# Performance work log

Measured on AMD Instinct MI355X. Metric: run time of the kernel, lower is better.

Reference implementation:

```python
import jax, jax.numpy as jnp
import numpy as np

B = 128                      # num_graphs (cell lines per batch)
SIZES = [706, 512, 256, 128] # nodes per graph at each level; final_node = 128
DIM = 256                    # dim_cell
DEG = 8                      # avg degree of gene-gene network
EPS = 1e-5                   # BatchNorm eps


def _build_graph():
    """Build per-graph edges (incl. self-loops, as GATConv adds) and predefined
    cluster assignments per layer, coarsening edges exactly like PyG max_pool
    (remove self-loops + coalesce). Replicated across B graphs with offsets."""
    rng = np.random.default_rng(0)
    e = rng.integers(0, SIZES[0], size=(2, SIZES[0] * DEG))
    e = e[:, e[0] != e[1]]
    e = np.unique(e, axis=1)
    edges, clusters = [], []
    cur = e
    for i in range(3):
        n_cur, n_next = SIZES[i], SIZES[i + 1]
        sl = np.arange(n_cur)
        e_sl = np.concatenate([cur, np.stack([sl, sl])], axis=1)  # add self-loops
        off = np.arange(B) * n_cur
        eg = (e_sl[:, None, :] + off[None, :, None]).reshape(2, -1)
        edges.append(eg.astype(np.int32))
        cl = np.concatenate([np.arange(n_next), rng.integers(0, n_next, size=n_cur - n_next)])
        rng.shuffle(cl)  # surjective cluster assignment n_cur -> n_next
        clg = (cl[None, :] + (np.arange(B) * n_next)[:, None]).reshape(-1)
        clusters.append(clg.astype(np.int32))
        src, dst = cl[cur[0]], cl[cur[1]]
        m = src != dst                      # pool_edge: remove self-loops
        cur = np.unique(np.stack([src[m], dst[m]]), axis=1)  # coalesce
    return edges, clusters


def setup_inputs() -> dict:
    edges, clusters = _build_graph()
    key = jax.random.key(0)
    ks = jax.random.split(key, 16)
    d = {"x": jax.random.normal(ks[0], (B * SIZES[0], 3), jnp.float32)}
    ins = [3, DIM, DIM]
    for i in range(3):
        s = 1.0 / np.sqrt(ins[i])
        a = 1.0 / np.sqrt(DIM)
        d[f"W{i}"] = jax.random.normal(ks[1 + i], (ins[i], DIM), jnp.float32) * s
        d[f"asrc{i}"] = jax.random.normal(ks[4 + i], (DIM,), jnp.float32) * a
        d[f"adst{i}"] = jax.random.normal(ks[7 + i], (DIM,), jnp.float32) * a
        d[f"b{i}"] = jnp.zeros((DIM,), jnp.float32)
        d[f"edge{i}"] = jnp.asarray(edges[i])
        d[f"cluster{i}"] = jnp.asarray(clusters[i])
    return d


def _gat(x, edge, W, a_s, a_d, b):
    """PyG GATConv, heads=1, negative_slope=0.2 (self-loops pre-added in edge)."""
    N = x.shape[0]
    h = x @ W                                    # [N, D]
    src, dst = edge[0], edge[1]
    e = jax.nn.leaky_relu((h * a_s).sum(-1)[src] + (h * a_d).sum(-1)[dst], 0.2)
    m = jax.ops.segment_max(e, dst, num_segments=N)     # segment softmax (stable)
    ex = jnp.exp(e - m[dst])
    ssum = jax.ops.segment_sum(ex, dst, num_segments=N)
    alpha = ex / ssum[dst]
    out = jax.ops.segment_sum(h[src] * alpha[:, None], dst, num_segments=N)
    return out + b


def _forward(x, Ws, a_ss, a_ds, bs, edges, clusters):
    for i in range(3):
        x = jax.nn.relu(_gat(x, edges[i], Ws[i], a_ss[i], a_ds[i], bs[i]))
        # max_pool: scatter-max over predefined clusters (coarsen nodes)
        x = jax.ops.segment_max(x, clusters[i], num_segments=B * SIZES[i + 1])
        # BatchNorm1d(affine=False), training mode: biased batch stats
        mean = x.mean(0)
        var = x.var(0)
        x = (x - mean) * jax.lax.rsqrt(var + EPS)
    return x.reshape(B, SIZES[3] * DIM)


def reference(x, W0, W1, W2, asrc0, asrc1, asrc2, adst0, adst1, adst2,
              b0, b1, b2, edge0, edge1, edge2, cluster0, cluster1, cluster2):
    return _forward(x, (W0, W1, W2), (asrc0, asrc1, asrc2), (adst0, adst1, adst2),
                    (b0, b1, b2), (edge0, edge1, edge2), (cluster0, cluster1, cluster2))
```

## Files before the change

### kernel.cpp

```cpp
#include <hip/hip_runtime.h>
#include <hip/hip_fp16.h>

#define DIM 256
#define MAXMEM 16
#define MAXDEG 288
#define NSH 16

typedef _Float16 f16x8 __attribute__((ext_vector_type(8)));
typedef float f32x4 __attribute__((ext_vector_type(4)));

__device__ inline unsigned short f2h(float f) {
  return __half_as_ushort(__float2half_rn(f));
}
__device__ inline float h2f(unsigned short u) {
  return __half2float(__ushort_as_half(u));
}
__device__ inline __half2 hmax2_(__half2 a, __half2 b) {
  __half2 c;
  c.x = __hgt(a.x, b.x) ? a.x : b.x;
  c.y = __hgt(a.y, b.y) ? a.y : b.y;
  return c;
}


struct BktArgs {
  const int* esrc[3]; const int* edst[3]; const int* cl[3];
  int Eb[3]; int Nb[3]; int est[3];
  int* bdeg[3]; int* bccnt[3]; int* bebkt[3]; int* bcbkt[3];
};

__global__ __launch_bounds__(256) void l0_bucket(
    const float* __restrict__ x, const float* __restrict__ W,
    const float* __restrict__ asv, const float* __restrict__ adv,
    unsigned short* __restrict__ h, float* __restrict__ ssrc,
    float* __restrict__ sdst, int N, int Nb0, int l0Blocks, int bgx,
    BktArgs a) {
  if ((int)blockIdx.x >= l0Blocks) {
    int bb = blockIdx.x - l0Blocks;
    int L = bb / bgx;
    int i = (bb % bgx) * 256 + threadIdx.x;
    if (i < a.Eb[L]) {
      int d = a.edst[L][i];
      int slot = atomicAdd(&a.bdeg[L][d], 1);
      if (slot < a.est[L]) a.bebkt[L][d * a.est[L] + slot] = a.esrc[L][i];
    }
    if (i < a.Nb[L]) {
      int c = a.cl[L][i];
      int slot = atomicAdd(&a.bccnt[L][c], 1);
      if (slot < MAXMEM) a.bcbkt[L][c * MAXMEM + slot] = i;
    }
    return;
  }
  int wid = (blockIdx.x * 256 + threadIdx.x) >> 6;
  int lane = threadIdx.x & 63;
  if (wid >= N) return;
  int nb = wid >> 7, g = wid & 127;
  const float* xr = x + ((size_t)g * Nb0 + nb) * 3;
  float x0 = xr[0], x1 = xr[1], x2 = xr[2];
  int c = lane * 4;
  float4 w0 = *(const float4*)(W + c);
  float4 w1 = *(const float4*)(W + 256 + c);
  float4 w2 = *(const float4*)(W + 512 + c);
  float4 hv;
  hv.x = fmaf(x0, w0.x, fmaf(x1, w1.x, x2 * w2.x));
  hv.y = fmaf(x0, w0.y, fmaf(x1, w1.y, x2 * w2.y));
  hv.z = fmaf(x0, w0.z, fmaf(x1, w1.z, x2 * w2.z));
  hv.w = fmaf(x0, w0.w, fmaf(x1, w1.w, x2 * w2.w));
  ((ushort4*)(h + (size_t)wid * DIM))[lane] =
      make_ushort4(f2h(hv.x), f2h(hv.y), f2h(hv.z), f2h(hv.w));
  float4 a1 = ((const float4*)asv)[lane];
  float4 a2 = ((const float4*)adv)[lane];
  float d1 = hv.x * a1.x + hv.y * a1.y + hv.z * a1.z + hv.w * a1.w;
  float d2 = hv.x * a2.x + hv.y * a2.y + hv.z * a2.z + hv.w * a2.w;
  for (int o = 32; o > 0; o >>= 1) {
    d1 += __shfl_down(d1, o);
    d2 += __shfl_down(d2, o);
  }
  if (lane == 0) { ssrc[wid] = d1; sdst[wid] = d2; }
}

__global__ __launch_bounds__(256) void prep_k(
    const float* __restrict__ W, const float* __restrict__ stats,
    float invN, unsigned short* __restrict__ Wt, float* __restrict__ cvec) {
  int n = blockIdx.x;
  int k = threadIdx.x;
  float s = 0.f, q = 0.f;
#pragma unroll
  for (int sh = 0; sh < NSH; sh++) {
    s += stats[sh * 512 + k];
    q += stats[sh * 512 + 256 + k];
  }
  float mu = s * invN;
  float var = q * invN - mu * mu;
  float istd = rsqrtf(var + 1e-5f);
  float w = W[(size_t)k * 256 + n] * istd;
  Wt[(size_t)n * 256 + k] = f2h(w);
  __shared__ float red[256];
  red[k] = mu * w;
  __syncthreads();
  for (int sft = 128; sft > 0; sft >>= 1) {
    if (k < sft) red[k] += red[k + sft];
    __syncthreads();
  }
  if (k == 0) cvec[n] = -red[0];
}

__global__ __launch_bounds__(256) void gemm_mfma(
    const unsigned short* __restrict__ A, const unsigned short* __restrict__ Wt,
    const float* __restrict__ cvec, const float* __restrict__ asv,
    const float* __restrict__ adv, unsigned short* __restrict__ H,
    float* __restrict__ ssrc, float* __restrict__ sdst, int M) {
  __shared__ unsigned short Bs[256 * 128];
  int tid = threadIdx.x;
  int wave = tid >> 6, lane = tid & 63;
  int m0 = blockIdx.x * 128 + wave * 32;
  int row = lane & 15, quad = lane >> 4;
  int swz = (row & 7) << 3;

  const unsigned short* Ap = A + (size_t)(m0 + row) * 256 + quad * 8;
  f32x4 acc[2][16] = {};

#pragma unroll
  for (int kh = 0; kh < 2; kh++) {
    if (kh) __syncthreads();
#pragma unroll
    for (int k = 0; k < 16; k++) {
      int c = k * 256 + tid;
      f16x8 v = *(const f16x8*)(const void*)(Wt + (size_t)(c >> 4) * 256 +
                                             kh * 128 + (c & 15) * 8);
      *(f16x8*)(void*)(&Bs[(c * 8) ^ (((c >> 4) & 7) << 3)]) = v;
    }
    __syncthreads();
#pragma unroll
    for (int j2 = 0; j2 < 4; j2++) {
      int j = kh * 4 + j2;
      f16x8 a0 = *(const f16x8*)(const void*)(Ap + j * 32);
      f16x8 a1 = *(const f16x8*)(const void*)(Ap + 16 * 256 + j * 32);
#pragma unroll
      for (int nt = 0; nt < 16; nt++) {
        f16x8 b = *(const f16x8*)(const void*)(
            &Bs[((nt * 16 + row) * 128 + j2 * 32 + quad * 8) ^ swz]);
        acc[0][nt] = __builtin_amdgcn_mfma_f32_16x16x32_f16(a0, b, acc[0][nt], 0, 0, 0);
        acc[1][nt] = __builtin_amdgcn_mfma_f32_16x16x32_f16(a1, b, acc[1][nt], 0, 0, 0);
      }
    }
  }

  float sav[16], sdv[16], cv[16];
#pragma unroll
  for (int nt = 0; nt < 16; nt++) {
    sav[nt] = asv[nt * 16 + row];
    sdv[nt] = adv[nt * 16 + row];
    cv[nt] = cvec[nt * 16 + row];
  }
#pragma unroll
  for (int sub = 0; sub < 2; sub++)
#pragma unroll
    for (int r = 0; r < 4; r++) {
      int mm = m0 + sub * 16 + quad * 4 + r;
      unsigned short* out = H + (size_t)mm * 256 + row;
      float d1 = 0.f, d2 = 0.f;
#pragma unroll
      for (int nt = 0; nt < 16; nt++) {
        float hv = acc[sub][nt][r] + cv[nt];
        out[nt * 16] = f2h(hv);
        d1 = fmaf(hv, sav[nt], d1);
        d2 = fmaf(hv, sdv[nt], d2);
      }
      for (int o = 1; o < 16; o <<= 1) {
        d1 += __shfl_xor(d1, o);
        d2 += __shfl_xor(d2, o);
      }
      if (row == 0) { ssrc[mm] = d1; sdst[mm] = d2; }
    }
}

__global__ __launch_bounds__(256) void gat_fused(
    const unsigned short* __restrict__ h, const int* __restrict__ bdeg,
    const int* __restrict__ bebkt, int estride,
    const int* __restrict__ bccnt, const int* __restrict__ bcbkt,
    const float* __restrict__ ssrc, const float* __restrict__ sdst,
    const float* __restrict__ bias, unsigned short* __restrict__ pooled,
    int Mb, int lgMb) {
  __shared__ float pLDS[MAXDEG * 8];
  __shared__ float psum[8];
  int b = blockIdx.x;
  int x = b & 7, t = b >> 3;
  int c = t & (Mb - 1);
  int set = x + 8 * (t >> lgMb);
  int tid = threadIdx.x;
  int gl = tid >> 5;
  int ch = tid & 31;
  int g = set * 8 + gl;
  int nm = bccnt[c]; if (nm > MAXMEM) nm = MAXMEM;
  float4 bf0 = *(const float4*)(bias + ch * 8);
  float4 bf1 = *(const float4*)(bias + ch * 8 + 4);
  __half2 hb[4] = {__floats2half2_rn(bf0.x, bf0.y), __floats2half2_rn(bf0.z, bf0.w),
                   __floats2half2_rn(bf1.x, bf1.y), __floats2half2_rn(bf1.z, bf1.w)};
  __half2 z = __float2half2_rn(0.f);
  __half2 best[4] = {z, z, z, z};
  for (int mi = 0; mi < nm; mi++) {
    int nb = __builtin_amdgcn_readfirstlane(bcbkt[c * MAXMEM + mi]);
    int deg = __builtin_amdgcn_readfirstlane(bdeg[nb]);
    if (deg > estride) deg = estride;
    const int* bk = bebkt + nb * estride;
    if (tid < 8) psum[tid] = 0.f;
    __syncthreads();
    for (int jj = tid; jj < deg * 8; jj += 256) {
      int j = jj >> 3, gi = jj & 7;
      int g2 = set * 8 + gi;
      int s = bk[j];
      float tt = ssrc[s * 128 + g2] + sdst[nb * 128 + g2];
      tt = tt > 0.f ? tt : 0.2f * tt;
      float p = __expf(tt);
      pLDS[jj] = p;
      atomicAdd(&psum[gi], p);
    }
    __syncthreads();
    float inv = 1.f / psum[gl];
    __half2 acc[4] = {z, z, z, z};
    int j = 0;
    for (; j + 4 <= deg; j += 4) {
      int4 ss = *(const int4*)(bk + j);
      __half2 hq0 = __float2half2_rn(pLDS[(j + 0) * 8 + gl] * inv);
      __half2 hq1 = __float2half2_rn(pLDS[(j + 1) * 8 + gl] * inv);
      __half2 hq2 = __float2half2_rn(pLDS[(j + 2) * 8 + gl] * inv);
      __half2 hq3 = __float2half2_rn(pLDS[(j + 3) * 8 + gl] * inv);
      uint4 v0 = *(const uint4*)(h + ((size_t)ss.x * 128 + g) * DIM + ch * 8);
      uint4 v1 = *(const uint4*)(h + ((size_t)ss.y * 128 + g) * DIM + ch * 8);
      uint4 v2 = *(const uint4*)(h + ((size_t)ss.z * 128 + g) * DIM + ch * 8);
      uint4 v3 = *(const uint4*)(h + ((size_t)ss.w * 128 + g) * DIM + ch * 8);
      union { uint4 u; __half2 p[4]; } u0, u1, u2, u3;
      u0.u = v0; u1.u = v1; u2.u = v2; u3.u = v3;
#pragma unroll
      for (int i = 0; i < 4; i++) {
        acc[i] = __hfma2(u0.p[i], hq0, acc[i]);
        acc[i] = __hfma2(u1.p[i], hq1, acc[i]);
        acc[i] = __hfma2(u2.p[i], hq2, acc[i]);
        acc[i] = __hfma2(u3.p[i], hq3, acc[i]);
      }
    }
    for (; j < deg; j++) {
      int s = bk[j];
      __half2 hq = __float2half2_rn(pLDS[j * 8 + gl] * inv);
      uint4 v0 = *(const uint4*)(h + ((size_t)s * 128 + g) * DIM + ch * 8);
      union { uint4 u; __half2 p[4]; } u0; u0.u = v0;
#pragma unroll
      for (int i = 0; i < 4; i++) acc[i] = __hfma2(u0.p[i], hq, acc[i]);
    }
#pragma unroll
    for (int i = 0; i < 4; i++)
      best[i] = hmax2_(best[i], __hadd2(acc[i], hb[i]));
    __syncthreads();
  }
  union { uint4 u; __half2 p[4]; } o;
#pragma unroll
  for (int i = 0; i < 4; i++) o.p[i] = best[i];
  *(uint4*)(pooled + ((size_t)c * 128 + g) * DIM + ch * 8) = o.u;
}

__global__ __launch_bounds__(256) void stats_k(
    const unsigned short* __restrict__ x, float* __restrict__ statL, int M) {
  int tid = threadIdx.x;
  int ch = tid & 31;
  int rg = tid >> 5;
  float s[8] = {}, q[8] = {};
  for (int r = blockIdx.x * 8 + rg; r < M; r += gridDim.x * 8) {
    uint4 v = *(const uint4*)(x + (size_t)r * DIM + ch * 8);
    union { uint4 u; __half2 p[4]; } uu; uu.u = v;
#pragma unroll
    for (int i = 0; i < 4; i++) {
      float2 f = __half22float2(uu.p[i]);
      s[2 * i]     += f.x; q[2 * i]     = fmaf(f.x, f.x, q[2 * i]);
      s[2 * i + 1] += f.y; q[2 * i + 1] = fmaf(f.y, f.y, q[2 * i + 1]);
    }
  }
  __shared__ float sm[512];
  sm[tid] = 0.f; sm[tid + 256] = 0.f;
  __syncthreads();
#pragma unroll
  for (int i = 0; i < 8; i++) {
    atomicAdd(&sm[ch * 8 + i], s[i]);
    atomicAdd(&sm[256 + ch * 8 + i], q[i]);
  }
  __syncthreads();
  float* sg = statL + (blockIdx.x & (NSH - 1)) * 512;
  atomicAdd(&sg[tid], sm[tid]);
  atomicAdd(&sg[tid + 256], sm[tid + 256]);
}

__global__ void norm_out(const unsigned short* __restrict__ xin,
                         float* __restrict__ xout,
                         const float* __restrict__ stats,
                         float invN, int Mb, int total) {
  int idx = blockIdx.x * 256 + threadIdx.x;
  if (idx >= total) return;
  int ch = idx & 255;
  int r = idx >> 8;
  int g = r & 127, c = r >> 7;
  float s = 0.f, q = 0.f;
#pragma unroll
  for (int sh = 0; sh < NSH; sh++) {
    s += stats[sh * 512 + ch];
    q += stats[sh * 512 + 256 + ch];
  }
  float mu = s * invN;
  float var = q * invN - mu * mu;
  float v = (h2f(xin[idx]) - mu) * rsqrtf(var + 1e-5f);
  xout[((size_t)g * Mb + c) * 256 + ch] = v;
}

extern "C" void kernel_launch(void* const* d_in, const int* in_sizes, int n_in,
                              void* d_out, int out_size, void* d_ws, size_t ws_size,
                              hipStream_t stream) {
  const int B = 128;
  const int Nb[4] = {706, 512, 256, 128};
  const int Ns[4] = {128 * 706, 128 * 512, 128 * 256, 128 * 128};
  const int lgMb[3] = {9, 8, 7};
  const int EST[3] = {64, 160, 288};

  int iW[3], iA[3], iD[3], iB_[3], iE[3], iC[3];
  if (in_sizes[2] == 256) {
    for (int i = 0; i < 3; i++) {
      iW[i] = 1 + 6 * i; iA[i] = 2 + 6 * i; iD[i] = 3 + 6 * i;
      iB_[i] = 4 + 6 * i; iE[i] = 5 + 6 * i; iC[i] = 6 + 6 * i;
    }
  } else {
    for (int i = 0; i < 3; i++) {
      iW[i] = 1 + i; iA[i] = 4 + i; iD[i] = 7 + i;
      iB_[i] = 10 + i; iE[i] = 13 + i; iC[i] = 16 + i;
    }
  }
  int E[3];
  for (int i = 0; i < 3; i++) E[i] = in_sizes[iE[i]] / 2;

  int bebktOff[3], bcbktOff[3];
  size_t bebktTot = 0, bcbktTot = 0;
  for (int i = 0; i < 3; i++) {
    bebktOff[i] = (int)bebktTot; bebktTot += (size_t)Nb[i] * EST[i];
    bcbktOff[i] = (int)bcbktTot; bcbktTot += (size_t)Nb[i + 1] * MAXMEM;
  }

  char* wsp = (char*)d_ws;
  size_t o = 0;
  auto alloc = [&](size_t bytes) -> void* {
    void* p = wsp + o;
    o = (o + bytes + 255) & ~(size_t)255;
    return p;
  };
  unsigned short* h      = (unsigned short*)alloc((size_t)Ns[0] * DIM * 2);
  unsigned short* pooled = (unsigned short*)alloc((size_t)Ns[1] * DIM * 2);
  float* ssrc   = (float*)alloc((size_t)Ns[0] * 4);
  float* sdst   = (float*)alloc((size_t)Ns[0] * 4);
  float* statbuf= (float*)alloc((size_t)3 * NSH * 512 * 4);
  int*   bmeta  = (int*)alloc((size_t)3 * (Nb[0] + Nb[1]) * 4);
  char*  zend   = wsp + o;
  int*   bebkt  = (int*)alloc(bebktTot * 4);
  int*   bcbkt  = (int*)alloc(bcbktTot * 4);
  unsigned short* Wt = (unsigned short*)alloc(256 * 256 * 2);
  float* cvec   = (float*)alloc(256 * 4);
  (void)ws_size; (void)n_in; (void)out_size;

  const float* xin = (const float*)d_in[0];

  hipMemsetAsync(statbuf, 0, (size_t)(zend - (char*)statbuf), stream);

  BktArgs ba;
  int maxG = 0;
  for (int L = 0; L < 3; L++) {
    int Eb = E[L] / B;
    ba.esrc[L] = (const int*)d_in[iE[L]];
    ba.edst[L] = ba.esrc[L] + E[L];
    ba.cl[L]   = (const int*)d_in[iC[L]];
    ba.Eb[L] = Eb; ba.Nb[L] = Nb[L]; ba.est[L] = EST[L];
    ba.bdeg[L]  = bmeta + L * (Nb[0] + Nb[1]);
    ba.bccnt[L] = ba.bdeg[L] + Nb[L];
    ba.bebkt[L] = bebkt + bebktOff[L];
    ba.bcbkt[L] = bcbkt + bcbktOff[L];
    int gneed = (Eb > Nb[L] ? Eb : Nb[L]);
    if (gneed > maxG) maxG = gneed;
  }
  int bgx = (maxG + 255) / 256;

  for (int L = 0; L < 3; L++) {
    int N = Ns[L], M = Ns[L + 1];
    int NbL = Nb[L];
    const float* W  = (const float*)d_in[iW[L]];
    const float* av = (const float*)d_in[iA[L]];
    const float* dv = (const float*)d_in[iD[L]];
    const float* bv = (const float*)d_in[iB_[L]];
    float* statL = statbuf + (size_t)L * NSH * 512;
    int* bdeg = bmeta + L * (Nb[0] + Nb[1]);
    int* bccnt = bdeg + NbL;
    int* beb = bebkt + bebktOff[L];
    int* bcb = bcbkt + bcbktOff[L];

    if (L == 0) {
      int l0Blocks = (N + 3) / 4;
      l0_bucket<<<l0Blocks + bgx * 3, 256, 0, stream>>>(
          xin, W, av, dv, h, ssrc, sdst, N, NbL, l0Blocks, bgx, ba);
    } else {
      float* pstat = statbuf + (size_t)(L - 1) * NSH * 512;
      prep_k<<<256, 256, 0, stream>>>(W, pstat, 1.0f / (float)N, Wt, cvec);
      gemm_mfma<<<N / 128, 256, 0, stream>>>(pooled, Wt, cvec, av, dv,
                                             h, ssrc, sdst, N);
    }

    int MbL = Nb[L + 1];
    gat_fused<<<MbL * 16, 256, 0, stream>>>(h, bdeg, beb, EST[L], bccnt, bcb,
                                            ssrc, sdst, bv, pooled,
                                            MbL, lgMb[L]);

    stats_k<<<512, 256, 0, stream>>>(pooled, statL, M);
  }

  norm_out<<<((size_t)Ns[3] * DIM + 255) / 256, 256, 0, stream>>>(
      pooled, (float*)d_out, statbuf + (size_t)2 * NSH * 512,
      1.0f / (float)Ns[3], Nb[3], Ns[3] * DIM);
}
```

Measured before the change: 326.0 us.

## Double-buffer attention scores and replace LDS atomics with wave-shuffle sums

In the fused GAT aggregate and pool kernel, the attention-score and exp stage for the next cluster member now runs while the current member is aggregated. It writes into a second LDS buffer, which cuts the barriers per member from two to one. The per-group softmax denominator is now summed with wave shuffles into per-wave partial slots instead of LDS atomicAdd. The cost is more LDS use per block, which may lower occupancy, and somewhat more complex control flow.

```diff
diff --git a/kernel.cpp b/kernel.cpp
--- a/kernel.cpp
+++ b/kernel.cpp
@@ -182,13 +182,14 @@
     const float* __restrict__ ssrc, const float* __restrict__ sdst,
     const float* __restrict__ bias, unsigned short* __restrict__ pooled,
     int Mb, int lgMb) {
-  __shared__ float pLDS[MAXDEG * 8];
-  __shared__ float psum[8];
+  __shared__ float pLDS[2][MAXDEG * 8];
+  __shared__ float psumW[2][32];
   int b = blockIdx.x;
   int x = b & 7, t = b >> 3;
   int c = t & (Mb - 1);
   int set = x + 8 * (t >> lgMb);
   int tid = threadIdx.x;
+  int wave = tid >> 6, lane = tid & 63;
   int gl = tid >> 5;
   int ch = tid & 31;
   int g = set * 8 + gl;
@@ -199,33 +200,54 @@
                    __floats2half2_rn(bf1.x, bf1.y), __floats2half2_rn(bf1.z, bf1.w)};
   __half2 z = __float2half2_rn(0.f);
   __half2 best[4] = {z, z, z, z};
-  for (int mi = 0; mi < nm; mi++) {
-    int nb = __builtin_amdgcn_readfirstlane(bcbkt[c * MAXMEM + mi]);
-    int deg = __builtin_amdgcn_readfirstlane(bdeg[nb]);
-    if (deg > estride) deg = estride;
+
+  auto score = [&](int bi, int nb, int deg) {
+    float part = 0.f;
     const int* bk = bebkt + nb * estride;
-    if (tid < 8) psum[tid] = 0.f;
-    __syncthreads();
     for (int jj = tid; jj < deg * 8; jj += 256) {
       int j = jj >> 3, gi = jj & 7;
-      int g2 = set * 8 + gi;
       int s = bk[j];
-      float tt = ssrc[s * 128 + g2] + sdst[nb * 128 + g2];
+      float tt = ssrc[s * 128 + set * 8 + gi] + sdst[nb * 128 + set * 8 + gi];
       tt = tt > 0.f ? tt : 0.2f * tt;
       float p = __expf(tt);
-      pLDS[jj] = p;
-      atomicAdd(&psum[gi], p);
-    }
+      pLDS[bi][jj] = p;
+      part += p;
+    }
+    part += __shfl_xor(part, 8);
+    part += __shfl_xor(part, 16);
+    part += __shfl_xor(part, 32);
+    if (lane < 8) psumW[bi][wave * 8 + lane] = part;
+  };
+
+  int nbC = 0, degC = 0;
+  if (nm > 0) {
+    nbC = __builtin_amdgcn_readfirstlane(bcbkt[c * MAXMEM]);
+    degC = __builtin_amdgcn_readfirstlane(bdeg[nbC]);
+    if (degC > estride) degC = estride;
+    score(0, nbC, degC);
+  }
+  for (int mi = 0; mi < nm; mi++) {
     __syncthreads();
-    float inv = 1.f / psum[gl];
+    int nbN = 0, degN = 0;
+    if (mi + 1 < nm) {
+      nbN = __builtin_amdgcn_readfirstlane(bcbkt[c * MAXMEM + mi + 1]);
+      degN = __builtin_amdgcn_readfirstlane(bdeg[nbN]);
+      if (degN > estride) degN = estride;
+      score((mi + 1) & 1, nbN, degN);
+    }
+    int bi = mi & 1;
+    const float* pl = pLDS[bi];
+    float inv = 1.f / (psumW[bi][gl] + psumW[bi][8 + gl] +
+                       psumW[bi][16 + gl] + psumW[bi][24 + gl]);
+    const int* bk = bebkt + nbC * estride;
     __half2 acc[4] = {z, z, z, z};
     int j = 0;
-    for (; j + 4 <= deg; j += 4) {
+    for (; j + 4 <= degC; j += 4) {
       int4 ss = *(const int4*)(bk + j);
-      __half2 hq0 = __float2half2_rn(pLDS[(j + 0) * 8 + gl] * inv);
-      __half2 hq1 = __float2half2_rn(pLDS[(j + 1) * 8 + gl] * inv);
-      __half2 hq2 = __float2half2_rn(pLDS[(j + 2) * 8 + gl] * inv);
-      __half2 hq3 = __float2half2_rn(pLDS[(j + 3) * 8 + gl] * inv);
+      __half2 hq0 = __float2half2_rn(pl[(j + 0) * 8 + gl] * inv);
+      __half2 hq1 = __float2half2_rn(pl[(j + 1) * 8 + gl] * inv);
+      __half2 hq2 = __float2half2_rn(pl[(j + 2) * 8 + gl] * inv);
+      __half2 hq3 = __float2half2_rn(pl[(j + 3) * 8 + gl] * inv);
       uint4 v0 = *(const uint4*)(h + ((size_t)ss.x * 128 + g) * DIM + ch * 8);
       uint4 v1 = *(const uint4*)(h + ((size_t)ss.y * 128 + g) * DIM + ch * 8);
       uint4 v2 = *(const uint4*)(h + ((size_t)ss.z * 128 + g) * DIM + ch * 8);
@@ -240,9 +262,9 @@
         acc[i] = __hfma2(u3.p[i], hq3, acc[i]);
       }
     }
-    for (; j < deg; j++) {
+    for (; j < degC; j++) {
       int s = bk[j];
-      __half2 hq = __float2half2_rn(pLDS[j * 8 + gl] * inv);
+      __half2 hq = __float2half2_rn(pl[j * 8 + gl] * inv);
       uint4 v0 = *(const uint4*)(h + ((size_t)s * 128 + g) * DIM + ch * 8);
       union { uint4 u; __half2 p[4]; } u0; u0.u = v0;
 #pragma unroll
@@ -251,7 +273,7 @@
 #pragma unroll
     for (int i = 0; i < 4; i++)
       best[i] = hmax2_(best[i], __hadd2(acc[i], hb[i]));
-    __syncthreads();
+    nbC = nbN; degC = degN;
   }
   union { uint4 u; __half2 p[4]; } o;
 #pragma unroll
```

Result: faster. 318.2 us, median of 2 (-2.4%).
